# Optimization experiments

Measured on AMD Instinct MI355X. Metric: run time of the kernel, lower is better.

Reference implementation:

```python
import jax, jax.numpy as jnp
import numpy as np

N = 50000      # nodes
E = 800000     # edges (before self-loops)
D = 128        # input_dim
H = 128        # hidden_dim
G = 256        # graphs in batch


def setup_inputs() -> dict:
    key = jax.random.key(0)
    ks = jax.random.split(key, 6)
    x = jax.random.normal(ks[0], (N, D), dtype=jnp.float32)
    edge_index = jax.random.randint(ks[1], (2, E), 0, N, dtype=jnp.int32)
    batch = jnp.sort(jax.random.randint(ks[2], (N,), 0, G, dtype=jnp.int32))
    W1 = jax.random.normal(ks[3], (D, H), dtype=jnp.float32) / np.sqrt(D).astype(np.float32)
    b1 = jnp.zeros((H,), jnp.float32)
    W2 = jax.random.normal(ks[4], (H, H), dtype=jnp.float32) / np.sqrt(H).astype(np.float32)
    b2 = jnp.zeros((H,), jnp.float32)
    alpha = jnp.full((H,), 0.25, jnp.float32)  # PReLU(hidden_dim) init
    return dict(x=x, edge_index=edge_index, batch=batch,
                W1=W1, b1=b1, W2=W2, b2=b2, alpha=alpha)


def _gcn_layer(z, W, b, src, dst, norm):
    # GCNConv: z' = D^{-1/2}(A+I)D^{-1/2} (z W) + b
    zw = z @ W                                            # [N,H] dense GEMM
    agg = jnp.zeros_like(zw).at[dst].add(norm[:, None] * zw[src])  # scatter-add over edges
    return agg + b


def reference(x, edge_index, batch, W1, b1, W2, b2, alpha):
    loop = jnp.arange(N, dtype=edge_index.dtype)
    src = jnp.concatenate([edge_index[0], loop])          # add self-loops
    dst = jnp.concatenate([edge_index[1], loop])
    deg = jnp.zeros((N,), x.dtype).at[dst].add(jnp.float32(1.0))
    dinv = jnp.where(deg > 0, jax.lax.rsqrt(deg), 0.0)
    norm = dinv[src] * dinv[dst]                          # [E+N] edge weights

    zs = []
    z = x
    for (W, b) in ((W1, b1), (W2, b2)):
        z = _gcn_layer(z, W, b, src, dst, norm)
        z = jnp.where(z > 0, z, alpha * z)                # channel-wise PReLU (shared)
        zs.append(z)

    gs = [jax.ops.segment_sum(zi, batch, num_segments=G) for zi in zs]  # global_add_pool
    g = jnp.concatenate(gs, axis=1)                       # [G, num_layers*H]
    return z, g
```

## Files before the change

### kernel.cpp

```cpp
#include <hip/hip_runtime.h>
#include <stdint.h>


#define CAP 96

typedef __attribute__((ext_vector_type(8))) short short8;
typedef __attribute__((ext_vector_type(4))) float f32x4;

__device__ __forceinline__ uint16_t bf16rne(float f) {
    uint32_t u = __float_as_uint(f);
    uint32_t r = (u + 0x7fffu + ((u >> 16) & 1u)) >> 16;
    return (uint16_t)r;
}
__device__ __forceinline__ float bf_lo(uint32_t v) { return __uint_as_float(v << 16); }
__device__ __forceinline__ float bf_hi(uint32_t v) { return __uint_as_float(v & 0xffff0000u); }

__global__ __launch_bounds__(512) void k0(int* __restrict__ cursor, int nbC, int N,
                                          const float* __restrict__ W1,
                                          const float* __restrict__ W2,
                                          uint16_t* __restrict__ Wf1,
                                          uint16_t* __restrict__ Wf2,
                                          float* __restrict__ g_out, int nbZ,
                                          uint32_t* __restrict__ zw, int SL) {
    int bid = blockIdx.x, t = threadIdx.x;
    if (bid < nbC) {
        int i = bid * 512 + t;
        if (i <= N) cursor[i] = 0;
        if (bid == 0 && t < 64)
            zw[(size_t)(t >> 4) * SL + (size_t)N * 16 + (t & 15)] = 0u;
    } else if (bid < nbC + 8) {
        int tid = (bid - nbC) * 512 + t;
        const float* W = (tid & 2048) ? W2 : W1;
        uint16_t* O = (tid & 2048) ? Wf2 : Wf1;
        int q16 = tid & 2047;
        int lane = q16 & 63, n0ks = q16 >> 6;
        int n0 = n0ks >> 2, ks = n0ks & 3;
        int m = lane & 15, quad = lane >> 4;
        int nn = n0 * 16 + m;
        int kkb = ks * 32 + quad * 8;
        uint16_t v[8];
#pragma unroll
        for (int j = 0; j < 8; ++j) v[j] = bf16rne(W[(kkb + j) * 128 + nn]);
        *(short8*)&O[q16 * 8] = *(short8*)v;
    } else {
        int idx = (bid - nbC - 8) * 512 + t;
        ((float4*)g_out)[idx] = make_float4(0.f, 0.f, 0.f, 0.f);
    }
}

__device__ __forceinline__ void gemm_body(const float* Xf, const uint16_t* Xb,
                                          const uint16_t* __restrict__ Wf,
                                          uint16_t* __restrict__ Y, int nrows,
                                          const int* __restrict__ cnt,
                                          uint16_t* Wl, int bid, int t, int ySL) {
    int lane = t & 63, w = t >> 6;
    int row0 = bid * 128;
    for (int c = t; c < 2048; c += 512)
        *(short8*)&Wl[c * 8] = *(const short8*)&Wf[c * 8];
    int m = lane & 15, quad = lane >> 4;
    int arow = row0 + w * 16 + m;
    bool rowok = arow < nrows;
    short8 a[4];
    short8 zer = {0, 0, 0, 0, 0, 0, 0, 0};
    if (Xb) {
        const uint16_t* aptr = Xb + (size_t)arow * 128 + quad * 8;
#pragma unroll
        for (int ks = 0; ks < 4; ++ks)
            a[ks] = rowok ? *(const short8*)(aptr + ks * 32) : zer;
    } else {
        const float* ap = Xf + (size_t)arow * 128 + quad * 8;
#pragma unroll
        for (int ks = 0; ks < 4; ++ks) {
            if (rowok) {
                float4 u0 = *(const float4*)(ap + ks * 32);
                float4 u1 = *(const float4*)(ap + ks * 32 + 4);
                uint32_t q[4];
                q[0] = (uint32_t)bf16rne(u0.x) | ((uint32_t)bf16rne(u0.y) << 16);
                q[1] = (uint32_t)bf16rne(u0.z) | ((uint32_t)bf16rne(u0.w) << 16);
                q[2] = (uint32_t)bf16rne(u1.x) | ((uint32_t)bf16rne(u1.y) << 16);
                q[3] = (uint32_t)bf16rne(u1.z) | ((uint32_t)bf16rne(u1.w) << 16);
                a[ks] = *(short8*)q;
            } else a[ks] = zer;
        }
    }
    __syncthreads();

    f32x4 acc[8];
#pragma unroll
    for (int i = 0; i < 8; ++i) acc[i] = (f32x4){0.f, 0.f, 0.f, 0.f};
#pragma unroll
    for (int ks = 0; ks < 4; ++ks)
#pragma unroll
        for (int n0 = 0; n0 < 8; ++n0) {
            short8 b = *(short8*)&Wl[((n0 * 4 + ks) * 64 + lane) * 8];
            acc[n0] = __builtin_amdgcn_mfma_f32_16x16x32_bf16(a[ks], b, acc[n0], 0, 0, 0);
        }
    __syncthreads();

    float dsc[4] = {1.f, 1.f, 1.f, 1.f};
    if (cnt) {
#pragma unroll
        for (int r = 0; r < 4; ++r) {
            int gr = row0 + w * 16 + quad * 4 + r;
            int d = (gr < nrows) ? cnt[gr] : 0;
            dsc[r] = rsqrtf((float)(d + 1));
        }
    }

    uint16_t* Ep = Wl;
#pragma unroll
    for (int n0 = 0; n0 < 8; ++n0)
#pragma unroll
        for (int r = 0; r < 4; ++r)
            Ep[(w * 16 + quad * 4 + r) * 136 + n0 * 16 + m] = bf16rne(acc[n0][r] * dsc[r]);
    for (int r16 = 0; r16 < 16; ++r16) {
        int row = row0 + w * 16 + r16;
        if (row < nrows) {
            uint32_t v = *(uint32_t*)&Ep[(w * 16 + r16) * 136 + lane * 2];
            if (ySL)
                ((uint32_t*)Y)[(size_t)(lane >> 4) * ySL + (size_t)row * 16 + (lane & 15)] = v;
            else
                ((uint32_t*)Y)[(size_t)row * 64 + lane] = v;
        }
    }
}

__device__ __forceinline__ void fill_body(const int* __restrict__ src, const int* __restrict__ dst,
                                          int* __restrict__ cursor, uint16_t* __restrict__ col,
                                          int E, int fb, int t) {
    int base = fb * 2048 + t;
    int d[4], s[4], p[4];
#pragma unroll
    for (int k = 0; k < 4; ++k) {
        int e = base + k * 512;
        d[k] = (e < E) ? dst[e] : -1;
        s[k] = (e < E) ? src[e] : 0;
    }
#pragma unroll
    for (int k = 0; k < 4; ++k) if (d[k] >= 0) p[k] = atomicAdd(&cursor[d[k]], 1);
#pragma unroll
    for (int k = 0; k < 4; ++k)
        if (d[k] >= 0 && p[k] < CAP) col[(size_t)d[k] * CAP + p[k]] = (uint16_t)s[k];
}

__global__ __launch_bounds__(512, 8) void k5(const float* __restrict__ X,
                                             const uint16_t* __restrict__ Wf,
                                             uint16_t* __restrict__ Y, int nrows, int gemmGrid,
                                             const int* __restrict__ src, const int* __restrict__ dst,
                                             int* __restrict__ cursor, uint16_t* __restrict__ col,
                                             int E, int fillGrid, int SL) {
    __shared__ uint16_t Wl[17408];
    int bid = blockIdx.x, t = threadIdx.x;
    int mn = min(gemmGrid, fillGrid), mn2 = 2 * mn;
    int role, idx;
    if (bid < mn2) { role = bid & 1; idx = bid >> 1; }
    else { role = (gemmGrid > fillGrid) ? 0 : 1; idx = bid - mn2 + mn; }
    if (role == 0) gemm_body(X, nullptr, Wf, Y, nrows, nullptr, Wl, idx, t, SL);
    else fill_body(src, dst, cursor, col, E, idx, t);
}

__global__ __launch_bounds__(512, 8) void gemm2k(const uint16_t* __restrict__ Xb,
                                                 const uint16_t* __restrict__ Wf,
                                                 uint16_t* __restrict__ Y, int nrows,
                                                 const int* __restrict__ cnt, int SL) {
    __shared__ uint16_t Wl[17408];
    gemm_body(nullptr, Xb, Wf, Y, nrows, cnt, Wl, blockIdx.x, threadIdx.x, SL);
}

template <bool PS>
__global__ __launch_bounds__(256) void aggp(const uint32_t* __restrict__ zw,
                                            const int* __restrict__ cnt,
                                            const uint16_t* __restrict__ col,
                                            const float* __restrict__ bias,
                                            const float* __restrict__ alpha,
                                            const int* __restrict__ batch,
                                            float* __restrict__ gout, int col_off,
                                            uint32_t* __restrict__ z1b,
                                            float* __restrict__ zoutf,
                                            int mode, int n, int SL, int NB) {
    __shared__ int gsh[16];
    __shared__ float red[4][32];
    int bid = blockIdx.x;
    int s = (bid & 7) >> 1;
    int j = ((bid >> 3) << 1) | (bid & 1);
    if (j >= NB) return;
    int t = threadIdx.x;
    int wv = t >> 6, lane = t & 63;
    int g = lane >> 4, i = lane & 15;
    int node = j * 16 + wv * 4 + g;
    bool valid = node < n;
    int nd = valid ? node : n;
    int ncl = valid ? node : (n - 1);
    const uint32_t* zs = zw + (size_t)s * SL;
    int deg = cnt[nd];
    float di = rsqrtf((float)(deg + 1));
    uint32_t sv = zs[(uint32_t)nd * 16 + i];
    float sw = PS ? 1.f : di;
    float ax = sw * bf_lo(sv), ay = sw * bf_hi(sv);
    float bx = 0.f, by = 0.f;
    int len = min(deg, CAP);
    int len8 = (len + 7) & ~7;
    int m1 = max(len8, __shfl_xor(len8, 16));
    int mx = __builtin_amdgcn_readfirstlane(max(m1, __shfl_xor(m1, 32)));
    int permbase = (lane & 48) << 2;
    const uint32_t* cbu = (const uint32_t*)col;

    for (int c0 = 0; c0 < mx; c0 += 32) {
        uint32_t cc = cbu[(uint32_t)ncl * (CAP / 2) + (c0 >> 1) + i];
        int top = min(mx - c0, 32);
        for (int e = 0; e < top; e += 8) {
            uint32_t q0 = (uint32_t)__builtin_amdgcn_ds_bpermute(permbase + (((e + 0) >> 1) << 2), (int)cc);
            uint32_t q1 = (uint32_t)__builtin_amdgcn_ds_bpermute(permbase + (((e + 2) >> 1) << 2), (int)cc);
            uint32_t q2 = (uint32_t)__builtin_amdgcn_ds_bpermute(permbase + (((e + 4) >> 1) << 2), (int)cc);
            uint32_t q3 = (uint32_t)__builtin_amdgcn_ds_bpermute(permbase + (((e + 6) >> 1) << 2), (int)cc);
            int jj = c0 + e;
            int s0 = (jj + 0 < len) ? (int)(q0 & 0xffffu) : n;
            int s1 = (jj + 1 < len) ? (int)(q0 >> 16)     : n;
            int s2 = (jj + 2 < len) ? (int)(q1 & 0xffffu) : n;
            int s3 = (jj + 3 < len) ? (int)(q1 >> 16)     : n;
            int s4 = (jj + 4 < len) ? (int)(q2 & 0xffffu) : n;
            int s5 = (jj + 5 < len) ? (int)(q2 >> 16)     : n;
            int s6 = (jj + 6 < len) ? (int)(q3 & 0xffffu) : n;
            int s7 = (jj + 7 < len) ? (int)(q3 >> 16)     : n;
            uint32_t v0 = zs[(uint32_t)s0 * 16 + i];
            uint32_t v1 = zs[(uint32_t)s1 * 16 + i];
            uint32_t v2 = zs[(uint32_t)s2 * 16 + i];
            uint32_t v3 = zs[(uint32_t)s3 * 16 + i];
            uint32_t v4 = zs[(uint32_t)s4 * 16 + i];
            uint32_t v5 = zs[(uint32_t)s5 * 16 + i];
            uint32_t v6 = zs[(uint32_t)s6 * 16 + i];
            uint32_t v7 = zs[(uint32_t)s7 * 16 + i];
            float w0 = PS ? 1.f : rsqrtf((float)(cnt[s0] + 1));
            float w1 = PS ? 1.f : rsqrtf((float)(cnt[s1] + 1));
            float w2 = PS ? 1.f : rsqrtf((float)(cnt[s2] + 1));
            float w3 = PS ? 1.f : rsqrtf((float)(cnt[s3] + 1));
            float w4 = PS ? 1.f : rsqrtf((float)(cnt[s4] + 1));
            float w5 = PS ? 1.f : rsqrtf((float)(cnt[s5] + 1));
            float w6 = PS ? 1.f : rsqrtf((float)(cnt[s6] + 1));
            float w7 = PS ? 1.f : rsqrtf((float)(cnt[s7] + 1));
            ax += w0 * bf_lo(v0); ay += w0 * bf_hi(v0);
            bx += w1 * bf_lo(v1); by += w1 * bf_hi(v1);
            ax += w2 * bf_lo(v2); ay += w2 * bf_hi(v2);
            bx += w3 * bf_lo(v3); by += w3 * bf_hi(v3);
            ax += w4 * bf_lo(v4); ay += w4 * bf_hi(v4);
            bx += w5 * bf_lo(v5); by += w5 * bf_hi(v5);
            ax += w6 * bf_lo(v6); ay += w6 * bf_hi(v6);
            bx += w7 * bf_lo(v7); by += w7 * bf_hi(v7);
        }
    }
    ax += bx; ay += by;
    float2 bb = ((const float2*)bias)[s * 16 + i];
    float2 aa = ((const float2*)alpha)[s * 16 + i];
    float zx = di * ax + bb.x;
    float zy = di * ay + bb.y;
    zx = zx > 0.f ? zx : aa.x * zx;
    zy = zy > 0.f ? zy : aa.y * zy;

    if (valid) {
        if (mode == 0) {
            uint32_t pk = (uint32_t)bf16rne(zx) | ((uint32_t)bf16rne(zy) << 16);
            z1b[(size_t)node * 64 + s * 16 + i] = pk;
        } else {
            ((float2*)zoutf)[(size_t)node * 64 + s * 16 + i] = make_float2(zx, zy);
        }
    }

    int gr = valid ? batch[nd] : -1;
    if (i == 0) gsh[wv * 4 + g] = gr;
    __syncthreads();
    int g0 = gsh[0];
    bool uni = true;
#pragma unroll
    for (int q = 1; q < 16; ++q) uni &= (gsh[q] == g0);
    float cx = valid ? zx : 0.f, cy = valid ? zy : 0.f;
    if (uni) {
        float r1x = cx + __shfl_xor(cx, 16), r1y = cy + __shfl_xor(cy, 16);
        float r2x = r1x + __shfl_xor(r1x, 32), r2y = r1y + __shfl_xor(r1y, 32);
        if (lane < 16) { red[wv][2 * i] = r2x; red[wv][2 * i + 1] = r2y; }
        __syncthreads();
        if (wv == 0 && lane < 16) {
            float sx = red[0][2 * i] + red[1][2 * i] + red[2][2 * i] + red[3][2 * i];
            float sy = red[0][2 * i + 1] + red[1][2 * i + 1] + red[2][2 * i + 1] + red[3][2 * i + 1];
            float* base = &gout[(size_t)g0 * 256 + col_off + s * 32 + 2 * i];
            atomicAdd(&base[0], sx);
            atomicAdd(&base[1], sy);
        }
    } else {
        if (valid) {
            float* base = &gout[(size_t)gr * 256 + col_off + s * 32 + 2 * i];
            atomicAdd(&base[0], cx);
            atomicAdd(&base[1], cy);
        }
    }
}

extern "C" void kernel_launch(void* const* d_in, const int* in_sizes, int n_in,
                              void* d_out, int out_size, void* d_ws, size_t ws_size,
                              hipStream_t stream) {
    const float* x     = (const float*)d_in[0];
    const int*   eidx  = (const int*)d_in[1];
    const int*   batch = (const int*)d_in[2];
    const float* W1    = (const float*)d_in[3];
    const float* b1    = (const float*)d_in[4];
    const float* W2    = (const float*)d_in[5];
    const float* b2    = (const float*)d_in[6];
    const float* alpha = (const float*)d_in[7];

    const int N = in_sizes[2];
    const int E = in_sizes[1] / 2;
    const int G = (out_size - N * 128) / 256;

    const int* src = eidx;
    const int* dst = eidx + E;

    char* ws = (char*)d_ws;
    size_t off = 0;
    auto alloc = [&](size_t bytes) { void* q = ws + off; off = (off + bytes + 255) & ~(size_t)255; return q; };
    int*      cursor = (int*)alloc((size_t)(N + 1) * 4);
    uint16_t* col    = (uint16_t*)alloc((size_t)N * CAP * 2);
    uint32_t* zw     = (uint32_t*)alloc((size_t)(N + 1) * 128 * 2);
    uint32_t* z1b    = (uint32_t*)alloc((size_t)N * 128 * 2);
    uint16_t* Wf1    = (uint16_t*)alloc(128 * 128 * 2);
    uint16_t* Wf2    = (uint16_t*)alloc(128 * 128 * 2);

    float* z_out = (float*)d_out;
    float* g_out = (float*)d_out + (size_t)N * 128;

    const int SL = (N + 1) * 16;
    int nbC      = (N + 512) / 512;
    int nbZ      = (G * 256 / 4 + 511) / 512;
    int fillGrid = (E + 2047) / 2048;
    int gemmGrid = (N + 127) / 128;
    int NB       = (N + 15) / 16;
    int NBpad    = (NB + 1) & ~1;
    int aggGrid  = NBpad * 4;

    k0<<<nbC + 8 + nbZ, 512, 0, stream>>>(cursor, nbC, N, W1, W2, Wf1, Wf2, g_out, nbZ, zw, SL);
    k5<<<gemmGrid + fillGrid, 512, 0, stream>>>(x, Wf1, (uint16_t*)zw, N, gemmGrid,
                                                src, dst, cursor, col, E, fillGrid, SL);
    aggp<false><<<aggGrid, 256, 0, stream>>>(zw, cursor, col, b1, alpha, batch,
                                             g_out, 0, z1b, nullptr, 0, N, SL, NB);
    gemm2k<<<gemmGrid, 512, 0, stream>>>((const uint16_t*)z1b, Wf2, (uint16_t*)zw, N, cursor, SL);
    aggp<true><<<aggGrid, 256, 0, stream>>>(zw, cursor, col, b2, alpha, batch,
                                            g_out, 128, nullptr, z_out, 1, N, SL, NB);
}
```

Before: 244.9 us.

## Assign one wavefront per node in aggregation with padded sentinel column lists

The aggregation kernel now gives each node a full wavefront. Its four 16-lane groups split that node's neighbor list and combine their partial sums with cross-lane shuffles, replacing the ds_bpermute broadcast scheme and the per-lane length masking. The column array is pre-filled with a sentinel node index, which points at a zero row in zw, so the padded tail entries need no bounds checks. The cost is four times more blocks, one extra large memset of the column buffer in the init kernel, and only a quarter of the lanes writing outputs.

```diff
diff --git a/kernel.cpp b/kernel.cpp
--- a/kernel.cpp
+++ b/kernel.cpp
@@ -21,7 +21,8 @@
                                           uint16_t* __restrict__ Wf1,
                                           uint16_t* __restrict__ Wf2,
                                           float* __restrict__ g_out, int nbZ,
-                                          uint32_t* __restrict__ zw, int SL) {
+                                          uint32_t* __restrict__ zw, int SL,
+                                          uint32_t* __restrict__ colw, int nColV) {
     int bid = blockIdx.x, t = threadIdx.x;
     if (bid < nbC) {
         int i = bid * 512 + t;
@@ -42,9 +43,15 @@
 #pragma unroll
         for (int j = 0; j < 8; ++j) v[j] = bf16rne(W[(kkb + j) * 128 + nn]);
         *(short8*)&O[q16 * 8] = *(short8*)v;
-    } else {
+    } else if (bid < nbC + 8 + nbZ) {
         int idx = (bid - nbC - 8) * 512 + t;
         ((float4*)g_out)[idx] = make_float4(0.f, 0.f, 0.f, 0.f);
+    } else {
+        int idx = (bid - nbC - 8 - nbZ) * 512 + t;
+        if (idx < nColV) {
+            uint32_t p = ((uint32_t)N & 0xffffu) | ((uint32_t)N << 16);
+            ((uint4*)colw)[idx] = make_uint4(p, p, p, p);
+        }
     }
 }
 
@@ -117,10 +124,7 @@
         int row = row0 + w * 16 + r16;
         if (row < nrows) {
             uint32_t v = *(uint32_t*)&Ep[(w * 16 + r16) * 136 + lane * 2];
-            if (ySL)
-                ((uint32_t*)Y)[(size_t)(lane >> 4) * ySL + (size_t)row * 16 + (lane & 15)] = v;
-            else
-                ((uint32_t*)Y)[(size_t)row * 64 + lane] = v;
+            ((uint32_t*)Y)[(size_t)(lane >> 4) * ySL + (size_t)row * 16 + (lane & 15)] = v;
         }
     }
 }
@@ -178,7 +182,7 @@
                                             uint32_t* __restrict__ z1b,
                                             float* __restrict__ zoutf,
                                             int mode, int n, int SL, int NB) {
-    __shared__ int gsh[16];
+    __shared__ int gsh[4];
     __shared__ float red[4][32];
     int bid = blockIdx.x;
     int s = (bid & 7) >> 1;
@@ -187,68 +191,50 @@
     int t = threadIdx.x;
     int wv = t >> 6, lane = t & 63;
     int g = lane >> 4, i = lane & 15;
-    int node = j * 16 + wv * 4 + g;
+    int node = j * 4 + wv;
     bool valid = node < n;
     int nd = valid ? node : n;
-    int ncl = valid ? node : (n - 1);
     const uint32_t* zs = zw + (size_t)s * SL;
     int deg = cnt[nd];
     float di = rsqrtf((float)(deg + 1));
     uint32_t sv = zs[(uint32_t)nd * 16 + i];
-    float sw = PS ? 1.f : di;
-    float ax = sw * bf_lo(sv), ay = sw * bf_hi(sv);
+    float selfw = (g == 0) ? (PS ? 1.f : di) : 0.f;
+    float ax = selfw * bf_lo(sv), ay = selfw * bf_hi(sv);
     float bx = 0.f, by = 0.f;
-    int len = min(deg, CAP);
-    int len8 = (len + 7) & ~7;
-    int m1 = max(len8, __shfl_xor(len8, 16));
-    int mx = __builtin_amdgcn_readfirstlane(max(m1, __shfl_xor(m1, 32)));
-    int permbase = (lane & 48) << 2;
-    const uint32_t* cbu = (const uint32_t*)col;
-
-    for (int c0 = 0; c0 < mx; c0 += 32) {
-        uint32_t cc = cbu[(uint32_t)ncl * (CAP / 2) + (c0 >> 1) + i];
-        int top = min(mx - c0, 32);
-        for (int e = 0; e < top; e += 8) {
-            uint32_t q0 = (uint32_t)__builtin_amdgcn_ds_bpermute(permbase + (((e + 0) >> 1) << 2), (int)cc);
-            uint32_t q1 = (uint32_t)__builtin_amdgcn_ds_bpermute(permbase + (((e + 2) >> 1) << 2), (int)cc);
-            uint32_t q2 = (uint32_t)__builtin_amdgcn_ds_bpermute(permbase + (((e + 4) >> 1) << 2), (int)cc);
-            uint32_t q3 = (uint32_t)__builtin_amdgcn_ds_bpermute(permbase + (((e + 6) >> 1) << 2), (int)cc);
-            int jj = c0 + e;
-            int s0 = (jj + 0 < len) ? (int)(q0 & 0xffffu) : n;
-            int s1 = (jj + 1 < len) ? (int)(q0 >> 16)     : n;
-            int s2 = (jj + 2 < len) ? (int)(q1 & 0xffffu) : n;
-            int s3 = (jj + 3 < len) ? (int)(q1 >> 16)     : n;
-            int s4 = (jj + 4 < len) ? (int)(q2 & 0xffffu) : n;
-            int s5 = (jj + 5 < len) ? (int)(q2 >> 16)     : n;
-            int s6 = (jj + 6 < len) ? (int)(q3 & 0xffffu) : n;
-            int s7 = (jj + 7 < len) ? (int)(q3 >> 16)     : n;
-            uint32_t v0 = zs[(uint32_t)s0 * 16 + i];
-            uint32_t v1 = zs[(uint32_t)s1 * 16 + i];
-            uint32_t v2 = zs[(uint32_t)s2 * 16 + i];
-            uint32_t v3 = zs[(uint32_t)s3 * 16 + i];
-            uint32_t v4 = zs[(uint32_t)s4 * 16 + i];
-            uint32_t v5 = zs[(uint32_t)s5 * 16 + i];
-            uint32_t v6 = zs[(uint32_t)s6 * 16 + i];
-            uint32_t v7 = zs[(uint32_t)s7 * 16 + i];
-            float w0 = PS ? 1.f : rsqrtf((float)(cnt[s0] + 1));
-            float w1 = PS ? 1.f : rsqrtf((float)(cnt[s1] + 1));
-            float w2 = PS ? 1.f : rsqrtf((float)(cnt[s2] + 1));
-            float w3 = PS ? 1.f : rsqrtf((float)(cnt[s3] + 1));
-            float w4 = PS ? 1.f : rsqrtf((float)(cnt[s4] + 1));
-            float w5 = PS ? 1.f : rsqrtf((float)(cnt[s5] + 1));
-            float w6 = PS ? 1.f : rsqrtf((float)(cnt[s6] + 1));
-            float w7 = PS ? 1.f : rsqrtf((float)(cnt[s7] + 1));
-            ax += w0 * bf_lo(v0); ay += w0 * bf_hi(v0);
-            bx += w1 * bf_lo(v1); by += w1 * bf_hi(v1);
-            ax += w2 * bf_lo(v2); ay += w2 * bf_hi(v2);
-            bx += w3 * bf_lo(v3); by += w3 * bf_hi(v3);
-            ax += w4 * bf_lo(v4); ay += w4 * bf_hi(v4);
-            bx += w5 * bf_lo(v5); by += w5 * bf_hi(v5);
-            ax += w6 * bf_lo(v6); ay += w6 * bf_hi(v6);
-            bx += w7 * bf_lo(v7); by += w7 * bf_hi(v7);
-        }
+    int len8 = (min(deg, CAP) + 7) & ~7;
+    const uint32_t* colp = (const uint32_t*)(col + (size_t)nd * CAP);
+    int e = 0;
+    for (; e + 16 <= len8; e += 16) {
+        uint32_t c0 = colp[(e >> 1) + g];
+        uint32_t c1 = colp[(e >> 1) + 4 + g];
+        int i0 = (int)(c0 & 0xffffu), i1 = (int)(c0 >> 16);
+        int i2 = (int)(c1 & 0xffffu), i3 = (int)(c1 >> 16);
+        uint32_t v0 = zs[(uint32_t)i0 * 16 + i];
+        uint32_t v1 = zs[(uint32_t)i1 * 16 + i];
+        uint32_t v2 = zs[(uint32_t)i2 * 16 + i];
+        uint32_t v3 = zs[(uint32_t)i3 * 16 + i];
+        float w0 = PS ? 1.f : rsqrtf((float)(cnt[i0] + 1));
+        float w1 = PS ? 1.f : rsqrtf((float)(cnt[i1] + 1));
+        float w2 = PS ? 1.f : rsqrtf((float)(cnt[i2] + 1));
+        float w3 = PS ? 1.f : rsqrtf((float)(cnt[i3] + 1));
+        ax += w0 * bf_lo(v0); ay += w0 * bf_hi(v0);
+        bx += w1 * bf_lo(v1); by += w1 * bf_hi(v1);
+        ax += w2 * bf_lo(v2); ay += w2 * bf_hi(v2);
+        bx += w3 * bf_lo(v3); by += w3 * bf_hi(v3);
+    }
+    if (e < len8) {
+        uint32_t c0 = colp[(e >> 1) + g];
+        int i0 = (int)(c0 & 0xffffu), i1 = (int)(c0 >> 16);
+        uint32_t v0 = zs[(uint32_t)i0 * 16 + i];
+        uint32_t v1 = zs[(uint32_t)i1 * 16 + i];
+        float w0 = PS ? 1.f : rsqrtf((float)(cnt[i0] + 1));
+        float w1 = PS ? 1.f : rsqrtf((float)(cnt[i1] + 1));
+        ax += w0 * bf_lo(v0); ay += w0 * bf_hi(v0);
+        bx += w1 * bf_lo(v1); by += w1 * bf_hi(v1);
     }
     ax += bx; ay += by;
+    ax += __shfl_xor(ax, 16); ay += __shfl_xor(ay, 16);
+    ax += __shfl_xor(ax, 32); ay += __shfl_xor(ay, 32);
     float2 bb = ((const float2*)bias)[s * 16 + i];
     float2 aa = ((const float2*)alpha)[s * 16 + i];
     float zx = di * ax + bb.x;
@@ -256,7 +242,7 @@
     zx = zx > 0.f ? zx : aa.x * zx;
     zy = zy > 0.f ? zy : aa.y * zy;
 
-    if (valid) {
+    if (valid && g == 0) {
         if (mode == 0) {
             uint32_t pk = (uint32_t)bf16rne(zx) | ((uint32_t)bf16rne(zy) << 16);
             z1b[(size_t)node * 64 + s * 16 + i] = pk;
@@ -265,28 +251,24 @@
         }
     }
 
-    int gr = valid ? batch[nd] : -1;
-    if (i == 0) gsh[wv * 4 + g] = gr;
+    int gr = valid ? batch[node] : -1 - wv;
+    if (lane == 0) gsh[wv] = gr;
     __syncthreads();
-    int g0 = gsh[0];
-    bool uni = true;
-#pragma unroll
-    for (int q = 1; q < 16; ++q) uni &= (gsh[q] == g0);
+    bool uni = (gsh[0] == gsh[1]) && (gsh[1] == gsh[2]) && (gsh[2] == gsh[3]);
     float cx = valid ? zx : 0.f, cy = valid ? zy : 0.f;
     if (uni) {
-        float r1x = cx + __shfl_xor(cx, 16), r1y = cy + __shfl_xor(cy, 16);
-        float r2x = r1x + __shfl_xor(r1x, 32), r2y = r1y + __shfl_xor(r1y, 32);
-        if (lane < 16) { red[wv][2 * i] = r2x; red[wv][2 * i + 1] = r2y; }
+        if (g == 0) { red[wv][2 * i] = cx; red[wv][2 * i + 1] = cy; }
         __syncthreads();
-        if (wv == 0 && lane < 16) {
+        if (wv == 0 && g == 0) {
             float sx = red[0][2 * i] + red[1][2 * i] + red[2][2 * i] + red[3][2 * i];
             float sy = red[0][2 * i + 1] + red[1][2 * i + 1] + red[2][2 * i + 1] + red[3][2 * i + 1];
-            float* base = &gout[(size_t)g0 * 256 + col_off + s * 32 + 2 * i];
+            float* base = &gout[(size_t)gsh[0] * 256 + col_off + s * 32 + 2 * i];
             atomicAdd(&base[0], sx);
             atomicAdd(&base[1], sy);
         }
     } else {
-        if (valid) {
+        __syncthreads();
+        if (valid && g == 0) {
             float* base = &gout[(size_t)gr * 256 + col_off + s * 32 + 2 * i];
             atomicAdd(&base[0], cx);
             atomicAdd(&base[1], cy);
@@ -329,13 +311,15 @@
     const int SL = (N + 1) * 16;
     int nbC      = (N + 512) / 512;
     int nbZ      = (G * 256 / 4 + 511) / 512;
+    int nColV    = (N * CAP * 2) / 16;
+    int nbP      = (nColV + 511) / 512;
     int fillGrid = (E + 2047) / 2048;
     int gemmGrid = (N + 127) / 128;
-    int NB       = (N + 15) / 16;
-    int NBpad    = (NB + 1) & ~1;
-    int aggGrid  = NBpad * 4;
-
-    k0<<<nbC + 8 + nbZ, 512, 0, stream>>>(cursor, nbC, N, W1, W2, Wf1, Wf2, g_out, nbZ, zw, SL);
+    int NB       = (N + 3) / 4;
+    int aggGrid  = 8 * ((NB + 1) / 2);
+
+    k0<<<nbC + 8 + nbZ + nbP, 512, 0, stream>>>(cursor, nbC, N, W1, W2, Wf1, Wf2,
+                                                g_out, nbZ, zw, SL, (uint32_t*)col, nColV);
     k5<<<gemmGrid + fillGrid, 512, 0, stream>>>(x, Wf1, (uint16_t*)zw, N, gemmGrid,
                                                 src, dst, cursor, col, E, fillGrid, SL);
     aggp<false><<<aggGrid, 256, 0, stream>>>(zw, cursor, col, b1, alpha, batch,
```

Measured after the change: 315.1 us. 1.29x slower.
